# Optimization experiments

Measured on AMD Instinct MI355X. Metric: run time of the kernel, lower is better.

Reference implementation:

```python
import jax, jax.numpy as jnp
import numpy as np

N, FP, H, E, B = 60000, 120, 512, 3, 600
NNZ = 5_000_000
NFORCE = 3 * N
ELEMENTS = jnp.array([1, 8, 29], dtype=jnp.int32)  # unique_atoms (H, O, Cu)


def setup_inputs():
    key = jax.random.key(0)
    ks = jax.random.split(key, 10)
    fingerprints = jax.random.normal(ks[0], (N, FP), jnp.float32)
    atomic_numbers = ELEMENTS[jax.random.randint(ks[1], (N,), 0, E)]
    image_idx = jnp.sort(jax.random.randint(ks[2], (N,), 0, B)).astype(jnp.int32)
    W1 = jax.random.normal(ks[3], (E, FP, H), jnp.float32) / np.float32(np.sqrt(FP))
    b1 = jnp.zeros((E, H), jnp.float32)
    W2 = jax.random.normal(ks[4], (E, H, H), jnp.float32) / np.float32(np.sqrt(H))
    b2 = jnp.zeros((E, H), jnp.float32)
    W3 = jax.random.normal(ks[5], (E, H, 1), jnp.float32) / np.float32(np.sqrt(H))
    b3 = jnp.zeros((E, 1), jnp.float32)
    # sparse fprimes [N*FP, 3*N] in COO form
    fprime_rows = jax.random.randint(ks[6], (NNZ,), 0, N * FP).astype(jnp.int32)
    fprime_cols = jax.random.randint(ks[7], (NNZ,), 0, NFORCE).astype(jnp.int32)
    fprime_vals = jax.random.normal(ks[8], (NNZ,), jnp.float32) * 0.01
    return {"fingerprints": fingerprints, "atomic_numbers": atomic_numbers,
            "image_idx": image_idx, "W1": W1, "b1": b1, "W2": W2, "b2": b2,
            "W3": W3, "b3": b3, "fprime_rows": fprime_rows,
            "fprime_cols": fprime_cols, "fprime_vals": fprime_vals}


def _energy(fingerprints, W1, b1, W2, b2, W3, b3, mask, image_idx):
    # stacked per-element 3-layer tanh MLPs, evaluated densely over all atoms
    h = jnp.tanh(jnp.einsum('nf,efh->enh', fingerprints, W1) + b1[:, None, :])
    h = jnp.tanh(jnp.einsum('enh,ehk->enk', h, W2) + b2[:, None, :])
    out = jnp.einsum('enh,eho->eno', h, W3) + b3[:, None, :]  # [E, N, 1]
    o = jnp.sum(mask.T * out[..., 0], axis=0)  # mask-select per-atom energy [N]
    return jax.ops.segment_sum(o, image_idx, num_segments=B)  # per-image energy [B]


def reference(fingerprints, atomic_numbers, image_idx, W1, b1, W2, b2, W3, b3,
              fprime_rows, fprime_cols, fprime_vals):
    # ElementMask: one-hot over unique atomic numbers
    mask = (atomic_numbers[:, None] == ELEMENTS[None, :]).astype(fingerprints.dtype)  # [N, E]
    efn = lambda fp: _energy(fp, W1, b1, W2, b2, W3, b3, mask, image_idx)
    energy, vjp_fn = jax.vjp(efn, fingerprints)
    # grad of energy wrt fingerprints with grad_outputs = ones
    g = vjp_fn(jnp.ones_like(energy))[0].reshape(-1)  # [N*FP]
    # forces = -fprimes^T @ g  via sparse scatter
    forces = -jax.ops.segment_sum(fprime_vals * g[fprime_rows], fprime_cols,
                                  num_segments=NFORCE).reshape(-1, 3)  # [N, 3]
    return (energy, forces)
```

## Files before the change

### kernel.cpp

```cpp
#include <hip/hip_runtime.h>

#define N_ATOMS 60000
#define FPD 120
#define HD 512
#define EE 3
#define BB 600
#define NNZ_C 5000000
#define NFORCE (3 * N_ATOMS)
#define TB 32
#define CBITS 12
#define NBUCK ((NFORCE + 4095) / 4096)
#define NSLOT 16
#define BCAP 118000
#define SCAT_BLOCKS ((NNZ_C / 4 + 4095) / 4096)
#define TPE 660

typedef unsigned short ushort_t;
typedef unsigned int uint_t;
typedef unsigned long long u64_t;
typedef __attribute__((ext_vector_type(8))) __bf16 bf16x8;
typedef __attribute__((ext_vector_type(4))) float f32x4;
typedef __attribute__((ext_vector_type(4))) int i32x4;

union BF8 { f32x4 f; bf16x8 h; };

__device__ __forceinline__ ushort_t f2bf(float x) {
    uint_t u = __builtin_bit_cast(uint_t, x);
    u = (u + 0x7FFFu + ((u >> 16) & 1u)) >> 16;
    return (ushort_t)u;
}
__device__ __forceinline__ float bf2f(ushort_t s) {
    uint_t u = ((uint_t)s) << 16;
    return __builtin_bit_cast(float, u);
}
__device__ __forceinline__ float fast_tanh(float x) {
    float e2 = __expf(2.f * x);
    return fmaf(-2.f, __frcp_rn(e2 + 1.f), 1.f);
}

__global__ __launch_bounds__(256) void build_lists(const int* __restrict__ z,
                                                   int* __restrict__ counts,
                                                   int* __restrict__ lists) {
    __shared__ int lc[3];
    __shared__ int lbase[3];
    const int t = threadIdx.x;
    if (t < 3) lc[t] = 0;
    __syncthreads();
    const int i = blockIdx.x * 256 + t;
    int e = 0, pos = 0;
    if (i < N_ATOMS) {
        int zi = z[i];
        e = (zi == 1) ? 0 : ((zi == 8) ? 1 : 2);
        pos = atomicAdd(&lc[e], 1);
    }
    __syncthreads();
    if (t < 3) lbase[t] = atomicAdd(&counts[t], lc[t]);
    __syncthreads();
    if (i < N_ATOMS) lists[e * N_ATOMS + lbase[e] + pos] = i;
}

#define R_W2 (EE * 16 * 32 * 512)
#define R_W1 (EE * 4 * 32 * 512)
#define R_W1T (EE * 16 * 8 * 512)
__global__ __launch_bounds__(256) void pack_all(
    const float* __restrict__ W1, const float* __restrict__ W2,
    ushort_t* __restrict__ W1p, ushort_t* __restrict__ W2p,
    ushort_t* __restrict__ W2Tp, ushort_t* __restrict__ W1Tp) {
    int idx = blockIdx.x * 256 + threadIdx.x;
    if (idx < R_W2) {
        int p = idx;
        int j = p & 7, L = (p >> 3) & 63, ct = (p >> 9) & 31, ks = (p >> 14) & 15, e = p >> 18;
        int k = ks * 32 + ((L >> 4) << 3) + j;
        int n = (ct << 4) + (L & 15);
        W2p[p]  = f2bf(W2[((e << 9) + k) * 512 + n]);
        W2Tp[p] = f2bf(W2[((e << 9) + n) * 512 + k]);
    } else if (idx < R_W2 + R_W1) {
        int p = idx - R_W2;
        int j = p & 7, L = (p >> 3) & 63, ct = (p >> 9) & 31, ks = (p >> 14) & 3, e = p >> 16;
        int k = ks * 32 + ((L >> 4) << 3) + j;
        int n = (ct << 4) + (L & 15);
        W1p[p] = (k < FPD) ? f2bf(W1[(e * FPD + k) * 512 + n]) : (ushort_t)0;
    } else if (idx < R_W2 + R_W1 + R_W1T) {
        int p = idx - R_W2 - R_W1;
        int j = p & 7, L = (p >> 3) & 63, ct = (p >> 9) & 7, ks = (p >> 12) & 15, e = p >> 16;
        int k = ks * 32 + ((L >> 4) << 3) + j;
        int n = (ct << 4) + (L & 15);
        W1Tp[p] = (n < FPD) ? f2bf(W1[(e * FPD + n) * 512 + k]) : (ushort_t)0;
    }
}

#define STR 520
#define FSTR 136

__global__ __launch_bounds__(512, 4) void mlp_mfma(
    const float* __restrict__ fps, const int* __restrict__ image_idx,
    const float* __restrict__ b1, const float* __restrict__ b2,
    const float* __restrict__ W3, const float* __restrict__ b3,
    const ushort_t* __restrict__ W1p, const ushort_t* __restrict__ W2p,
    const ushort_t* __restrict__ W2Tp, const ushort_t* __restrict__ W1Tp,
    const int* __restrict__ counts, const int* __restrict__ lists,
    float* __restrict__ energy, ushort_t* __restrict__ g,
    const int* __restrict__ rows, const int* __restrict__ cols,
    const float* __restrict__ vals, int* __restrict__ bcnt,
    u64_t* __restrict__ bpack, int scatBlocks) {
    __shared__ ushort_t sH1[TB * STR];
    __shared__ ushort_t sD[TB * STR];
    __shared__ float sW3[512];
    __shared__ float eAcc[TB];
    __shared__ int sAtom[TB];
    __shared__ int sImg[TB];
    __shared__ int sLcnt[NBUCK];
    __shared__ int sLcur[NBUCK];

    const int t = threadIdx.x;

    if (blockIdx.x < (uint_t)scatBlocks) {
        const int vk0 = blockIdx.x * 4096;
        if (t < NBUCK) sLcnt[t] = 0;
        __syncthreads();
        i32x4 cc[8];
#pragma unroll
        for (int i = 0; i < 8; i++) {
            int vk = vk0 + i * 512 + t;
            if (vk < NNZ_C / 4) {
                i32x4 c = __builtin_nontemporal_load((const i32x4*)cols + vk);
                cc[i] = c;
                atomicAdd(&sLcnt[c.x >> CBITS], 1);
                atomicAdd(&sLcnt[c.y >> CBITS], 1);
                atomicAdd(&sLcnt[c.z >> CBITS], 1);
                atomicAdd(&sLcnt[c.w >> CBITS], 1);
            } else {
                cc[i].x = -1;
            }
        }
        __syncthreads();
        if (t < NBUCK) sLcur[t] = t * BCAP + atomicAdd(&bcnt[t], sLcnt[t]);
        __syncthreads();
#pragma unroll
        for (int i = 0; i < 8; i++) {
            int vk = vk0 + i * 512 + t;
            if (cc[i].x != -1) {
                i32x4 r = __builtin_nontemporal_load((const i32x4*)rows + vk);
                f32x4 v = __builtin_nontemporal_load((const f32x4*)vals + vk);
                int rr[4] = {r.x, r.y, r.z, r.w};
                int ccv[4] = {cc[i].x, cc[i].y, cc[i].z, cc[i].w};
                float vv[4] = {v.x, v.y, v.z, v.w};
#pragma unroll
                for (int u = 0; u < 4; u++) {
                    int b = ccv[u] >> CBITS;
                    int pos = atomicAdd(&sLcur[b], 1);
                    u64_t pk = (u64_t)(uint_t)rr[u] |
                               ((u64_t)(uint_t)(ccv[u] & ((1 << CBITS) - 1)) << 23) |
                               ((u64_t)f2bf(vv[u]) << 35);
                    bpack[pos] = pk;
                }
            }
        }
        return;
    }

    const int mb = blockIdx.x - scatBlocks;
    const int e = mb / TPE;
    const int tile = mb - e * TPE;
    if (e >= EE) return;
    const int cnt = counts[e];
    const int base = tile * TB;
    if (base >= cnt) return;
    const int nA = min(TB, cnt - base);
    const int* lst = lists + e * N_ATOMS + base;

    const int w = t >> 6, lane = t & 63, quad = lane >> 4, lc = lane & 15;

    if (t < TB) {
        int a = (t < nA) ? lst[t] : -1;
        sAtom[t] = a;
        sImg[t] = (a >= 0) ? image_idx[a] : 0;
        eAcc[t] = 0.f;
    }
    if (t < 512) sW3[t] = W3[e * 512 + t];
    for (int i = t; i < TB * 128; i += 512) {
        int a = i >> 7, f = i & 127;
        float v = 0.f;
        if (f < FPD && a < nA) v = __builtin_nontemporal_load(&fps[(long long)lst[a] * FPD + f]);
        sD[a * FSTR + f] = f2bf(v);
    }
    __syncthreads();

    float b1c[4], b2c[4];
#pragma unroll
    for (int c = 0; c < 4; c++) {
        int col = w * 64 + c * 16 + lc;
        b1c[c] = b1[e * 512 + col];
        b2c[c] = b2[e * 512 + col];
    }

    f32x4 acc[2][4];
    float h1f[2][4][4];

#pragma unroll
    for (int rt = 0; rt < 2; rt++)
#pragma unroll
        for (int c = 0; c < 4; c++) acc[rt][c] = (f32x4)0.f;
    {
        const ushort_t* wbase = W1p + ((size_t)(e * 4) * 32 + w * 4) * 512 + lane * 8;
        BF8 bb[4][4];
#pragma unroll
        for (int ks = 0; ks < 4; ks++)
#pragma unroll
            for (int c = 0; c < 4; c++)
                bb[ks][c].f = *(const f32x4*)(wbase + ((size_t)ks * 32 + c) * 512);
#pragma unroll
        for (int ks = 0; ks < 4; ks++) {
            bf16x8 a0 = *(const bf16x8*)((const char*)sD + lc * (FSTR * 2) + ks * 64 + quad * 16);
            bf16x8 a1 = *(const bf16x8*)((const char*)sD + (16 + lc) * (FSTR * 2) + ks * 64 + quad * 16);
#pragma unroll
            for (int c = 0; c < 4; c++) {
                acc[0][c] = __builtin_amdgcn_mfma_f32_16x16x32_bf16(a0, bb[ks][c].h, acc[0][c], 0, 0, 0);
                acc[1][c] = __builtin_amdgcn_mfma_f32_16x16x32_bf16(a1, bb[ks][c].h, acc[1][c], 0, 0, 0);
            }
        }
    }
#pragma unroll
    for (int c = 0; c < 4; c++) {
        int col = w * 64 + c * 16 + lc;
#pragma unroll
        for (int rt = 0; rt < 2; rt++)
#pragma unroll
            for (int r = 0; r < 4; r++) {
                int row = rt * 16 + quad * 4 + r;
                float hv = fast_tanh(acc[rt][c][r] + b1c[c]);
                h1f[rt][c][r] = hv;
                sH1[row * STR + col] = f2bf(hv);
            }
    }
    __syncthreads();

#pragma unroll
    for (int rt = 0; rt < 2; rt++)
#pragma unroll
        for (int c = 0; c < 4; c++) acc[rt][c] = (f32x4)0.f;
    {
        const ushort_t* wbase = W2p + ((size_t)(e * 16) * 32 + w * 4) * 512 + lane * 8;
#pragma unroll
        for (int ksc = 0; ksc < 4; ksc++) {
            BF8 bb[4][4];
#pragma unroll
            for (int kk = 0; kk < 4; kk++)
#pragma unroll
                for (int c = 0; c < 4; c++)
                    bb[kk][c].f = *(const f32x4*)(wbase + (size_t)(ksc * 4 + kk) * 32 * 512 + (size_t)c * 512);
#pragma unroll
            for (int kk = 0; kk < 4; kk++) {
                int ks = ksc * 4 + kk;
                bf16x8 a0 = *(const bf16x8*)((const char*)sH1 + lc * (STR * 2) + ks * 64 + quad * 16);
                bf16x8 a1 = *(const bf16x8*)((const char*)sH1 + (16 + lc) * (STR * 2) + ks * 64 + quad * 16);
#pragma unroll
                for (int c = 0; c < 4; c++) {
                    acc[0][c] = __builtin_amdgcn_mfma_f32_16x16x32_bf16(a0, bb[kk][c].h, acc[0][c], 0, 0, 0);
                    acc[1][c] = __builtin_amdgcn_mfma_f32_16x16x32_bf16(a1, bb[kk][c].h, acc[1][c], 0, 0, 0);
                }
            }
        }
    }
    {
        float ep[2][4];
#pragma unroll
        for (int rt = 0; rt < 2; rt++)
#pragma unroll
            for (int r = 0; r < 4; r++) ep[rt][r] = 0.f;
#pragma unroll
        for (int c = 0; c < 4; c++) {
            int col = w * 64 + c * 16 + lc;
            float w3c = sW3[col];
#pragma unroll
            for (int rt = 0; rt < 2; rt++)
#pragma unroll
                for (int r = 0; r < 4; r++) {
                    int row = rt * 16 + quad * 4 + r;
                    float h2 = fast_tanh(acc[rt][c][r] + b2c[c]);
                    ep[rt][r] += h2 * w3c;
                    sD[row * STR + col] = f2bf(w3c * (1.f - h2 * h2));
                }
        }
#pragma unroll
        for (int rt = 0; rt < 2; rt++)
#pragma unroll
            for (int r = 0; r < 4; r++) {
                float p = ep[rt][r];
                p += __shfl_xor(p, 1);
                p += __shfl_xor(p, 2);
                p += __shfl_xor(p, 4);
                p += __shfl_xor(p, 8);
                if (lc == 0) atomicAdd(&eAcc[rt * 16 + quad * 4 + r], p);
            }
    }
    __syncthreads();

    if (t < nA) atomicAdd(&energy[sImg[t]], eAcc[t] + b3[e]);

#pragma unroll
    for (int rt = 0; rt < 2; rt++)
#pragma unroll
        for (int c = 0; c < 4; c++) acc[rt][c] = (f32x4)0.f;
    {
        const ushort_t* wbase = W2Tp + ((size_t)(e * 16) * 32 + w * 4) * 512 + lane * 8;
#pragma unroll
        for (int ksc = 0; ksc < 4; ksc++) {
            BF8 bb[4][4];
#pragma unroll
            for (int kk = 0; kk < 4; kk++)
#pragma unroll
                for (int c = 0; c < 4; c++)
                    bb[kk][c].f = *(const f32x4*)(wbase + (size_t)(ksc * 4 + kk) * 32 * 512 + (size_t)c * 512);
#pragma unroll
            for (int kk = 0; kk < 4; kk++) {
                int ks = ksc * 4 + kk;
                bf16x8 a0 = *(const bf16x8*)((const char*)sD + lc * (STR * 2) + ks * 64 + quad * 16);
                bf16x8 a1 = *(const bf16x8*)((const char*)sD + (16 + lc) * (STR * 2) + ks * 64 + quad * 16);
#pragma unroll
                for (int c = 0; c < 4; c++) {
                    acc[0][c] = __builtin_amdgcn_mfma_f32_16x16x32_bf16(a0, bb[kk][c].h, acc[0][c], 0, 0, 0);
                    acc[1][c] = __builtin_amdgcn_mfma_f32_16x16x32_bf16(a1, bb[kk][c].h, acc[1][c], 0, 0, 0);
                }
            }
        }
    }
#pragma unroll
    for (int c = 0; c < 4; c++)
#pragma unroll
        for (int rt = 0; rt < 2; rt++)
#pragma unroll
            for (int r = 0; r < 4; r++) {
                float hv = h1f[rt][c][r];
                acc[rt][c][r] *= (1.f - hv * hv);
            }
    __syncthreads();
#pragma unroll
    for (int c = 0; c < 4; c++) {
        int col = w * 64 + c * 16 + lc;
#pragma unroll
        for (int rt = 0; rt < 2; rt++)
#pragma unroll
            for (int r = 0; r < 4; r++) {
                int row = rt * 16 + quad * 4 + r;
                sH1[row * STR + col] = f2bf(acc[rt][c][r]);
            }
    }
    __syncthreads();

    f32x4 acc7[2];
#pragma unroll
    for (int rt = 0; rt < 2; rt++) acc7[rt] = (f32x4)0.f;
    {
        const ushort_t* wbase = W1Tp + ((size_t)(e * 16) * 8 + w) * 512 + lane * 8;
#pragma unroll
        for (int ksc = 0; ksc < 2; ksc++) {
            BF8 bb[8];
#pragma unroll
            for (int kk = 0; kk < 8; kk++)
                bb[kk].f = *(const f32x4*)(wbase + (size_t)(ksc * 8 + kk) * 8 * 512);
#pragma unroll
            for (int kk = 0; kk < 8; kk++) {
                int ks = ksc * 8 + kk;
                bf16x8 a0 = *(const bf16x8*)((const char*)sH1 + lc * (STR * 2) + ks * 64 + quad * 16);
                bf16x8 a1 = *(const bf16x8*)((const char*)sH1 + (16 + lc) * (STR * 2) + ks * 64 + quad * 16);
                acc7[0] = __builtin_amdgcn_mfma_f32_16x16x32_bf16(a0, bb[kk].h, acc7[0], 0, 0, 0);
                acc7[1] = __builtin_amdgcn_mfma_f32_16x16x32_bf16(a1, bb[kk].h, acc7[1], 0, 0, 0);
            }
        }
    }
    {
        int col = w * 16 + lc;
#pragma unroll
        for (int rt = 0; rt < 2; rt++)
#pragma unroll
            for (int r = 0; r < 4; r++) {
                int row = rt * 16 + quad * 4 + r;
                if (col < FPD && row < nA)
                    g[(long long)sAtom[row] * FPD + col] = f2bf(acc7[rt][r]);
            }
    }
}

__global__ __launch_bounds__(256) void scatter_lds_cap(
    const u64_t* __restrict__ bpack, const int* __restrict__ bcnt,
    const ushort_t* __restrict__ g, float* __restrict__ forcesP) {
    __shared__ float facc[1 << CBITS];
    const int b = blockIdx.x >> 4;
    const int s = blockIdx.x & (NSLOT - 1);
    const int t = threadIdx.x;
    for (int i = t; i < (1 << CBITS); i += 256) facc[i] = 0.f;
    __syncthreads();
    const int base = b * BCAP;
    const int end = base + bcnt[b];
    for (int i = base + s * 256 + t; i < end; i += NSLOT * 256) {
        u64_t pk = bpack[i];
        int r = (int)(pk & 0x7FFFFFu);
        int cin = (int)((pk >> 23) & 0xFFFu);
        float v = bf2f((ushort_t)(pk >> 35));
        atomicAdd(&facc[cin], -v * bf2f(g[r]));
    }
    __syncthreads();
    const int colbase = b << CBITS;
    float* fp = forcesP + (size_t)s * NFORCE;
    for (int i = t; i < (1 << CBITS); i += 256) {
        int col = colbase + i;
        if (col < NFORCE) __builtin_nontemporal_store(facc[i], &fp[col]);
    }
}

__global__ __launch_bounds__(256) void bucket_hist(const int* __restrict__ cols,
                                                   int* __restrict__ bcnt) {
    __shared__ int h[NBUCK];
    const int t = threadIdx.x;
    if (t < NBUCK) h[t] = 0;
    __syncthreads();
    const int nv = NNZ_C / 4;
    for (int vk = blockIdx.x * 256 + t; vk < nv; vk += gridDim.x * 256) {
        i32x4 c = __builtin_nontemporal_load((const i32x4*)cols + vk);
        atomicAdd(&h[c.x >> CBITS], 1);
        atomicAdd(&h[c.y >> CBITS], 1);
        atomicAdd(&h[c.z >> CBITS], 1);
        atomicAdd(&h[c.w >> CBITS], 1);
    }
    __syncthreads();
    if (t < NBUCK) atomicAdd(&bcnt[t], h[t]);
}

__global__ void bucket_scan(const int* __restrict__ bcnt, int* __restrict__ bbase,
                            int* __restrict__ bcur) {
    if (threadIdx.x == 0 && blockIdx.x == 0) {
        int s = 0;
        for (int i = 0; i < NBUCK; i++) { bbase[i] = s; bcur[i] = s; s += bcnt[i]; }
    }
}

__global__ __launch_bounds__(256) void bucket_scatter(
    const int* __restrict__ rows, const int* __restrict__ cols,
    const float* __restrict__ vals, int* __restrict__ bcur,
    u64_t* __restrict__ bpack) {
    __shared__ int lcnt[NBUCK];
    __shared__ int lcur[NBUCK];
    const int t = threadIdx.x;
    if (t < NBUCK) lcnt[t] = 0;
    __syncthreads();
    const int vk0 = blockIdx.x * 2048;
    i32x4 ccache[8];
    int nb[8][4];
#pragma unroll
    for (int i = 0; i < 8; i++) {
        int vk = vk0 + i * 256 + t;
        if (vk * 4 < NNZ_C) {
            i32x4 c = __builtin_nontemporal_load((const i32x4*)cols + vk);
            ccache[i] = c;
            nb[i][0] = c.x >> CBITS; nb[i][1] = c.y >> CBITS;
            nb[i][2] = c.z >> CBITS; nb[i][3] = c.w >> CBITS;
            atomicAdd(&lcnt[nb[i][0]], 1);
            atomicAdd(&lcnt[nb[i][1]], 1);
            atomicAdd(&lcnt[nb[i][2]], 1);
            atomicAdd(&lcnt[nb[i][3]], 1);
        } else {
            nb[i][0] = -1;
        }
    }
    __syncthreads();
    if (t < NBUCK) lcur[t] = atomicAdd(&bcur[t], lcnt[t]);
    __syncthreads();
#pragma unroll
    for (int i = 0; i < 8; i++) {
        int vk = vk0 + i * 256 + t;
        if (vk * 4 < NNZ_C) {
            i32x4 r = __builtin_nontemporal_load((const i32x4*)rows + vk);
            f32x4 v = __builtin_nontemporal_load((const f32x4*)vals + vk);
            int rr[4] = {r.x, r.y, r.z, r.w};
            int cc[4] = {ccache[i].x, ccache[i].y, ccache[i].z, ccache[i].w};
            float vv[4] = {v.x, v.y, v.z, v.w};
#pragma unroll
            for (int u = 0; u < 4; u++) {
                int pos = atomicAdd(&lcur[nb[i][u]], 1);
                u64_t pk = (u64_t)(uint_t)rr[u] |
                           ((u64_t)(uint_t)(cc[u] & ((1 << CBITS) - 1)) << 23) |
                           ((u64_t)f2bf(vv[u]) << 35);
                bpack[pos] = pk;
            }
        }
    }
}

__global__ __launch_bounds__(256) void scatter_lds(
    const u64_t* __restrict__ bpack, const int* __restrict__ bbase,
    const int* __restrict__ bcnt, const ushort_t* __restrict__ g,
    float* __restrict__ forcesP) {
    __shared__ float facc[1 << CBITS];
    const int b = blockIdx.x >> 4;
    const int s = blockIdx.x & (NSLOT - 1);
    const int t = threadIdx.x;
    for (int i = t; i < (1 << CBITS); i += 256) facc[i] = 0.f;
    __syncthreads();
    const int base = bbase[b];
    const int end = base + bcnt[b];
    for (int i = base + s * 256 + t; i < end; i += NSLOT * 256) {
        u64_t pk = bpack[i];
        int r = (int)(pk & 0x7FFFFFu);
        int cin = (int)((pk >> 23) & 0xFFFu);
        float v = bf2f((ushort_t)(pk >> 35));
        atomicAdd(&facc[cin], -v * bf2f(g[r]));
    }
    __syncthreads();
    const int colbase = b << CBITS;
    float* fp = forcesP + (size_t)s * NFORCE;
    for (int i = t; i < (1 << CBITS); i += 256) {
        int col = colbase + i;
        if (col < NFORCE) __builtin_nontemporal_store(facc[i], &fp[col]);
    }
}

__global__ void reduce_forces(const float* __restrict__ forcesP, float* __restrict__ forces) {
    int i = blockIdx.x * blockDim.x + threadIdx.x;
    if (i >= NFORCE) return;
    float s = 0.f;
#pragma unroll
    for (int x = 0; x < NSLOT; x++) s += forcesP[(size_t)x * NFORCE + i];
    forces[i] = s;
}

__global__ __launch_bounds__(256) void scatter_forces(
    const int* __restrict__ rows, const int* __restrict__ cols,
    const float* __restrict__ vals, const ushort_t* __restrict__ g,
    float* __restrict__ forcesP) {
    int k = blockIdx.x * 256 + threadIdx.x;
    if (k >= NNZ_C / 4) return;
    int slot = blockIdx.x & (NSLOT - 1);
    i32x4 r = __builtin_nontemporal_load((const i32x4*)rows + k);
    i32x4 c = __builtin_nontemporal_load((const i32x4*)cols + k);
    f32x4 v = __builtin_nontemporal_load((const f32x4*)vals + k);
    float* fp = forcesP + (size_t)slot * NFORCE;
    atomicAdd(&fp[c.x], -v.x * bf2f(g[r.x]));
    atomicAdd(&fp[c.y], -v.y * bf2f(g[r.y]));
    atomicAdd(&fp[c.z], -v.z * bf2f(g[r.z]));
    atomicAdd(&fp[c.w], -v.w * bf2f(g[r.w]));
}

extern "C" void kernel_launch(void* const* d_in, const int* in_sizes, int n_in,
                              void* d_out, int out_size, void* d_ws, size_t ws_size,
                              hipStream_t stream) {
    const float* fps = (const float*)d_in[0];
    const int* z = (const int*)d_in[1];
    const int* img = (const int*)d_in[2];
    const float* W1 = (const float*)d_in[3];
    const float* b1 = (const float*)d_in[4];
    const float* W2 = (const float*)d_in[5];
    const float* b2 = (const float*)d_in[6];
    const float* W3 = (const float*)d_in[7];
    const float* b3 = (const float*)d_in[8];
    const int* rows = (const int*)d_in[9];
    const int* cols = (const int*)d_in[10];
    const float* vals = (const float*)d_in[11];

    float* out = (float*)d_out;
    float* energy = out;
    float* forces = out + BB;

    char* ws = (char*)d_ws;
    int* counts = (int*)ws;
    int* lists = (int*)(ws + 256);
    ushort_t* W1p = (ushort_t*)(ws + 720384);
    ushort_t* W2p = (ushort_t*)(ws + 1113600);
    ushort_t* W2Tp = (ushort_t*)(ws + 2686464);
    ushort_t* W1Tp = (ushort_t*)(ws + 4259328);
    ushort_t* g = (ushort_t*)(ws + 4652544);
    float* forcesP = (float*)(ws + 19052544);
    int* bmeta = (int*)(ws + 30572544);
    int* bcnt = bmeta, *bbase = bmeta + 64, *bcur = bmeta + 128;
    u64_t* bpack = (u64_t*)(ws + 30573568);
    const size_t WS_FAST = 30573568ull + (size_t)NBUCK * BCAP * 8;
    const size_t WS_NEED = 70573568;
    (void)in_sizes; (void)n_in; (void)out_size;

    (void)hipMemsetAsync(energy, 0, BB * sizeof(float), stream);
    (void)hipMemsetAsync(counts, 0, 256, stream);

    build_lists<<<(N_ATOMS + 255) / 256, 256, 0, stream>>>(z, counts, lists);
    pack_all<<<(R_W2 + R_W1 + R_W1T + 255) / 256, 256, 0, stream>>>(
        W1, W2, W1p, W2p, W2Tp, W1Tp);

    int tiles = (N_ATOMS + TB - 1) / TB;

    if (ws_size >= WS_FAST) {
        (void)hipMemsetAsync(bmeta, 0, 768, stream);
        mlp_mfma<<<SCAT_BLOCKS + EE * TPE, 512, 0, stream>>>(
            fps, img, b1, b2, W3, b3, W1p, W2p, W2Tp, W1Tp,
            counts, lists, energy, g,
            rows, cols, vals, bcnt, bpack, SCAT_BLOCKS);
        scatter_lds_cap<<<NBUCK * NSLOT, 256, 0, stream>>>(bpack, bcnt, g, forcesP);
        reduce_forces<<<(NFORCE + 255) / 256, 256, 0, stream>>>(forcesP, forces);
    } else if (ws_size >= WS_NEED) {
        (void)hipMemsetAsync(bmeta, 0, 768, stream);
        mlp_mfma<<<EE * tiles, 512, 0, stream>>>(
            fps, img, b1, b2, W3, b3, W1p, W2p, W2Tp, W1Tp,
            counts, lists, energy, g,
            rows, cols, vals, bcnt, bpack, 0);
        bucket_hist<<<256, 256, 0, stream>>>(cols, bcnt);
        bucket_scan<<<1, 64, 0, stream>>>(bcnt, bbase, bcur);
        bucket_scatter<<<(NNZ_C + 8191) / 8192, 256, 0, stream>>>(
            rows, cols, vals, bcur, bpack);
        scatter_lds<<<NBUCK * NSLOT, 256, 0, stream>>>(bpack, bbase, bcnt, g, forcesP);
        reduce_forces<<<(NFORCE + 255) / 256, 256, 0, stream>>>(forcesP, forces);
    } else {
        (void)hipMemsetAsync(forcesP, 0, (size_t)NSLOT * NFORCE * sizeof(float), stream);
        mlp_mfma<<<EE * tiles, 512, 0, stream>>>(
            fps, img, b1, b2, W3, b3, W1p, W2p, W2Tp, W1Tp,
            counts, lists, energy, g,
            rows, cols, vals, bcnt, (u64_t*)forcesP , 0);
        scatter_forces<<<(NNZ_C / 4 + 255) / 256, 256, 0, stream>>>(rows, cols, vals, g, forcesP);
        reduce_forces<<<(NFORCE + 255) / 256, 256, 0, stream>>>(forcesP, forces);
    }
}
```

Baseline: 392.0 us.

## Fuse prep kernels, stagger MFMA k-order per wave, raise MFMA priority, drop barrier

Merges the atom-list build and weight-packing kernels into one launch to save a kernel launch. In the MLP kernel each wave starts its k-loop at a different offset, which spreads LDS bank and weight-load traffic across waves, and s_setprio raises wave priority around MFMA bursts. It also removes a __syncthreads between the W2T backward GEMM and the sH1 overwrite. That barrier removal risks a race, since other waves may still be reading sH1 in the preceding GEMM.

```diff
diff --git a/kernel.cpp b/kernel.cpp
--- a/kernel.cpp
+++ b/kernel.cpp
@@ -14,6 +14,7 @@
 #define BCAP 118000
 #define SCAT_BLOCKS ((NNZ_C / 4 + 4095) / 4096)
 #define TPE 660
+#define BL_BLOCKS ((N_ATOMS + 255) / 256)
 
 typedef unsigned short ushort_t;
 typedef unsigned int uint_t;
@@ -38,35 +39,34 @@
     return fmaf(-2.f, __frcp_rn(e2 + 1.f), 1.f);
 }
 
-__global__ __launch_bounds__(256) void build_lists(const int* __restrict__ z,
-                                                   int* __restrict__ counts,
-                                                   int* __restrict__ lists) {
-    __shared__ int lc[3];
-    __shared__ int lbase[3];
-    const int t = threadIdx.x;
-    if (t < 3) lc[t] = 0;
-    __syncthreads();
-    const int i = blockIdx.x * 256 + t;
-    int e = 0, pos = 0;
-    if (i < N_ATOMS) {
-        int zi = z[i];
-        e = (zi == 1) ? 0 : ((zi == 8) ? 1 : 2);
-        pos = atomicAdd(&lc[e], 1);
-    }
-    __syncthreads();
-    if (t < 3) lbase[t] = atomicAdd(&counts[t], lc[t]);
-    __syncthreads();
-    if (i < N_ATOMS) lists[e * N_ATOMS + lbase[e] + pos] = i;
-}
-
 #define R_W2 (EE * 16 * 32 * 512)
 #define R_W1 (EE * 4 * 32 * 512)
 #define R_W1T (EE * 16 * 8 * 512)
-__global__ __launch_bounds__(256) void pack_all(
+__global__ __launch_bounds__(256) void prep_all(
+    const int* __restrict__ z, int* __restrict__ counts, int* __restrict__ lists,
     const float* __restrict__ W1, const float* __restrict__ W2,
     ushort_t* __restrict__ W1p, ushort_t* __restrict__ W2p,
     ushort_t* __restrict__ W2Tp, ushort_t* __restrict__ W1Tp) {
-    int idx = blockIdx.x * 256 + threadIdx.x;
+    const int t = threadIdx.x;
+    if (blockIdx.x < BL_BLOCKS) {
+        __shared__ int lc[3];
+        __shared__ int lbase[3];
+        if (t < 3) lc[t] = 0;
+        __syncthreads();
+        const int i = blockIdx.x * 256 + t;
+        int e = 0, pos = 0;
+        if (i < N_ATOMS) {
+            int zi = z[i];
+            e = (zi == 1) ? 0 : ((zi == 8) ? 1 : 2);
+            pos = atomicAdd(&lc[e], 1);
+        }
+        __syncthreads();
+        if (t < 3) lbase[t] = atomicAdd(&counts[t], lc[t]);
+        __syncthreads();
+        if (i < N_ATOMS) lists[e * N_ATOMS + lbase[e] + pos] = i;
+        return;
+    }
+    int idx = (blockIdx.x - BL_BLOCKS) * 256 + t;
     if (idx < R_W2) {
         int p = idx;
         int j = p & 7, L = (p >> 3) & 63, ct = (p >> 9) & 31, ks = (p >> 14) & 15, e = p >> 18;
@@ -210,14 +210,17 @@
             for (int c = 0; c < 4; c++)
                 bb[ks][c].f = *(const f32x4*)(wbase + ((size_t)ks * 32 + c) * 512);
 #pragma unroll
-        for (int ks = 0; ks < 4; ks++) {
+        for (int ks0 = 0; ks0 < 4; ks0++) {
+            int ks = (ks0 + w) & 3;
             bf16x8 a0 = *(const bf16x8*)((const char*)sD + lc * (FSTR * 2) + ks * 64 + quad * 16);
             bf16x8 a1 = *(const bf16x8*)((const char*)sD + (16 + lc) * (FSTR * 2) + ks * 64 + quad * 16);
+            __builtin_amdgcn_s_setprio(1);
 #pragma unroll
             for (int c = 0; c < 4; c++) {
                 acc[0][c] = __builtin_amdgcn_mfma_f32_16x16x32_bf16(a0, bb[ks][c].h, acc[0][c], 0, 0, 0);
                 acc[1][c] = __builtin_amdgcn_mfma_f32_16x16x32_bf16(a1, bb[ks][c].h, acc[1][c], 0, 0, 0);
             }
+            __builtin_amdgcn_s_setprio(0);
         }
     }
 #pragma unroll
@@ -242,7 +245,8 @@
     {
         const ushort_t* wbase = W2p + ((size_t)(e * 16) * 32 + w * 4) * 512 + lane * 8;
 #pragma unroll
-        for (int ksc = 0; ksc < 4; ksc++) {
+        for (int ksc0 = 0; ksc0 < 4; ksc0++) {
+            int ksc = (ksc0 + w) & 3;
             BF8 bb[4][4];
 #pragma unroll
             for (int kk = 0; kk < 4; kk++)
@@ -254,11 +258,13 @@
                 int ks = ksc * 4 + kk;
                 bf16x8 a0 = *(const bf16x8*)((const char*)sH1 + lc * (STR * 2) + ks * 64 + quad * 16);
                 bf16x8 a1 = *(const bf16x8*)((const char*)sH1 + (16 + lc) * (STR * 2) + ks * 64 + quad * 16);
+                __builtin_amdgcn_s_setprio(1);
 #pragma unroll
                 for (int c = 0; c < 4; c++) {
                     acc[0][c] = __builtin_amdgcn_mfma_f32_16x16x32_bf16(a0, bb[kk][c].h, acc[0][c], 0, 0, 0);
                     acc[1][c] = __builtin_amdgcn_mfma_f32_16x16x32_bf16(a1, bb[kk][c].h, acc[1][c], 0, 0, 0);
                 }
+                __builtin_amdgcn_s_setprio(0);
             }
         }
     }
@@ -305,7 +311,8 @@
     {
         const ushort_t* wbase = W2Tp + ((size_t)(e * 16) * 32 + w * 4) * 512 + lane * 8;
 #pragma unroll
-        for (int ksc = 0; ksc < 4; ksc++) {
+        for (int ksc0 = 0; ksc0 < 4; ksc0++) {
+            int ksc = (ksc0 + w) & 3;
             BF8 bb[4][4];
 #pragma unroll
             for (int kk = 0; kk < 4; kk++)
@@ -317,11 +324,13 @@
                 int ks = ksc * 4 + kk;
                 bf16x8 a0 = *(const bf16x8*)((const char*)sD + lc * (STR * 2) + ks * 64 + quad * 16);
                 bf16x8 a1 = *(const bf16x8*)((const char*)sD + (16 + lc) * (STR * 2) + ks * 64 + quad * 16);
+                __builtin_amdgcn_s_setprio(1);
 #pragma unroll
                 for (int c = 0; c < 4; c++) {
                     acc[0][c] = __builtin_amdgcn_mfma_f32_16x16x32_bf16(a0, bb[kk][c].h, acc[0][c], 0, 0, 0);
                     acc[1][c] = __builtin_amdgcn_mfma_f32_16x16x32_bf16(a1, bb[kk][c].h, acc[1][c], 0, 0, 0);
                 }
+                __builtin_amdgcn_s_setprio(0);
             }
         }
     }
@@ -334,7 +343,6 @@
                 float hv = h1f[rt][c][r];
                 acc[rt][c][r] *= (1.f - hv * hv);
             }
-    __syncthreads();
 #pragma unroll
     for (int c = 0; c < 4; c++) {
         int col = w * 64 + c * 16 + lc;
@@ -354,7 +362,8 @@
     {
         const ushort_t* wbase = W1Tp + ((size_t)(e * 16) * 8 + w) * 512 + lane * 8;
 #pragma unroll
-        for (int ksc = 0; ksc < 2; ksc++) {
+        for (int ksc0 = 0; ksc0 < 2; ksc0++) {
+            int ksc = (ksc0 + w) & 1;
             BF8 bb[8];
 #pragma unroll
             for (int kk = 0; kk < 8; kk++)
@@ -364,8 +373,10 @@
                 int ks = ksc * 8 + kk;
                 bf16x8 a0 = *(const bf16x8*)((const char*)sH1 + lc * (STR * 2) + ks * 64 + quad * 16);
                 bf16x8 a1 = *(const bf16x8*)((const char*)sH1 + (16 + lc) * (STR * 2) + ks * 64 + quad * 16);
+                __builtin_amdgcn_s_setprio(1);
                 acc7[0] = __builtin_amdgcn_mfma_f32_16x16x32_bf16(a0, bb[kk].h, acc7[0], 0, 0, 0);
                 acc7[1] = __builtin_amdgcn_mfma_f32_16x16x32_bf16(a1, bb[kk].h, acc7[1], 0, 0, 0);
+                __builtin_amdgcn_s_setprio(0);
             }
         }
     }
@@ -580,9 +591,9 @@
     (void)hipMemsetAsync(energy, 0, BB * sizeof(float), stream);
     (void)hipMemsetAsync(counts, 0, 256, stream);
 
-    build_lists<<<(N_ATOMS + 255) / 256, 256, 0, stream>>>(z, counts, lists);
-    pack_all<<<(R_W2 + R_W1 + R_W1T + 255) / 256, 256, 0, stream>>>(
-        W1, W2, W1p, W2p, W2Tp, W1Tp);
+    const int PACK_BLOCKS = (R_W2 + R_W1 + R_W1T + 255) / 256;
+    prep_all<<<BL_BLOCKS + PACK_BLOCKS, 256, 0, stream>>>(
+        z, counts, lists, W1, W2, W1p, W2p, W2Tp, W1Tp);
 
     int tiles = (N_ATOMS + TB - 1) / TB;
 
```

Measured after the change: 530.9 us. 35.4% more time.
